# Kernel optimization log

Hardware: AMD Instinct MI355X
Metric: run time of the kernel (lower is better)

Reference implementation:

```python
import jax, jax.numpy as jnp
import numpy as np

D = 1024
H = 16
DH = D // H  # 64

def setup_inputs() -> dict:
    key = jax.random.key(0)
    ks = jax.random.split(key, 9)
    B, L = 2, 2048
    s = 1.0 / np.sqrt(D)
    inp = {
        'x':  jax.random.normal(ks[0], (B, L, D), dtype=jnp.float32),
        'Wq': jax.random.uniform(ks[1], (D, D), jnp.float32, -s, s),
        'bq': jnp.zeros((D,), jnp.float32),
        'Wk': jax.random.uniform(ks[2], (D, D), jnp.float32, -s, s),
        'bk': jnp.zeros((D,), jnp.float32),
        'Wv': jax.random.uniform(ks[3], (D, D), jnp.float32, -s, s),
        'bv': jnp.zeros((D,), jnp.float32),
        'Wo': jax.random.uniform(ks[4], (D, D), jnp.float32, -s, s),
        'bo': jnp.zeros((D,), jnp.float32),
    }
    return inp

def reference(x, Wq, bq, Wk, bk, Wv, bv, Wo, bo):
    B, L, _ = x.shape
    # projections (torch Linear: x @ W.T + b; here weights stored as [D_in, D_out])
    q = (x @ Wq + bq).reshape(B, L, H, DH).transpose(0, 2, 1, 3)  # [B,H,L,DH]
    k = (x @ Wk + bk).reshape(B, L, H, DH).transpose(0, 2, 1, 3)
    v = (x @ Wv + bv).reshape(B, L, H, DH).transpose(0, 2, 1, 3)
    scores = jnp.einsum('bhqd,bhkd->bhqk', q, k) / jnp.sqrt(jnp.float32(DH))
    attn = jax.nn.softmax(scores, axis=-1)  # dropout p=0 / eval -> identity
    out = jnp.einsum('bhqk,bhkd->bhqd', attn, v)
    out = out.transpose(0, 2, 1, 3).reshape(B, L, D)
    return out @ Wo + bo
```

## Files before the change

kernel.cpp:

```cpp
#include <hip/hip_runtime.h>
#include <stdint.h>

typedef __attribute__((ext_vector_type(8)))  __bf16 bf16x8;
typedef __attribute__((ext_vector_type(4)))  __bf16 bf16x4;
typedef __attribute__((ext_vector_type(4)))  float  f32x4;
typedef __attribute__((ext_vector_type(16))) float  f32x16;
typedef __attribute__((ext_vector_type(4)))  int    i32x4;

#define DEV static __device__ __forceinline__

DEV float fast_exp2(float x) {
#if __has_builtin(__builtin_amdgcn_exp2f)
  return __builtin_amdgcn_exp2f(x);
#else
  return exp2f(x);
#endif
}

DEV uint32_t pack_bf2(float a, float b) {
  __bf16 x = (__bf16)a, y = (__bf16)b;
  uint16_t xu = __builtin_bit_cast(uint16_t, x);
  uint16_t yu = __builtin_bit_cast(uint16_t, y);
  return (uint32_t)xu | ((uint32_t)yu << 16);
}

DEV void gload_lds16(const void* g, void* l) {
  __builtin_amdgcn_global_load_lds(
      (const __attribute__((address_space(1))) void*)(uintptr_t)(g),
      (__attribute__((address_space(3))) void*)(uint32_t)(uintptr_t)(l),
      16, 0, 0);
}

#define SM_SCALE 0.18033688f

__global__ void k_prep(const float* __restrict__ x,  __bf16* __restrict__ xb,
                       const float* __restrict__ Wq, const float* __restrict__ Wk,
                       const float* __restrict__ Wv, const float* __restrict__ Wo,
                       __bf16* __restrict__ wtq, __bf16* __restrict__ wot) {
  const int z = blockIdx.z;
  if (z < 4) {
    const float* W  = (z == 0) ? Wq : (z == 1) ? Wk : (z == 2) ? Wv : Wo;
    __bf16*      Wt = (z == 3) ? wot : (wtq + (size_t)z * 1024 * 1024);
    __shared__ __bf16 T[64][66];
    int t = threadIdx.x;
    int r = t >> 2;
    int cq = (t & 3) << 4;
    {
      int gk = blockIdx.y * 64 + r;
      int gn0 = blockIdx.x * 64 + cq;
      const float* src = W + (size_t)gk * 1024 + gn0;
#pragma unroll
      for (int j = 0; j < 16; j += 4) {
        f32x4 v = *(const f32x4*)(src + j);
#pragma unroll
        for (int jj = 0; jj < 4; ++jj) T[r][cq + j + jj] = (__bf16)v[jj];
      }
    }
    __syncthreads();
    {
      int gn = blockIdx.x * 64 + r;
      int gk0 = blockIdx.y * 64 + cq;
      __bf16* dst = Wt + (size_t)gn * 1024 + gk0;
      bf16x8 o0, o1;
#pragma unroll
      for (int j = 0; j < 8; ++j) { o0[j] = T[cq + j][r]; o1[j] = T[cq + 8 + j][r]; }
      *(bf16x8*)dst = o0;
      *(bf16x8*)(dst + 8) = o1;
    }
  } else {
    int lb = (z - 4) * 256 + blockIdx.y * 16 + blockIdx.x;
    int i = (lb * 256 + (int)threadIdx.x) * 4;
    if (i < 4096 * 1024) {
      f32x4 v = *(const f32x4*)(x + i);
      bf16x4 o;
      o[0] = (__bf16)v[0]; o[1] = (__bf16)v[1];
      o[2] = (__bf16)v[2]; o[3] = (__bf16)v[3];
      *(bf16x4*)(xb + i) = o;
    }
  }
}

__global__ void k_vt(const __bf16* __restrict__ qkv, __bf16* __restrict__ kvf) {
  int lt = blockIdx.x, bh = blockIdx.y;
  int b = bh >> 4, h = bh & 15;
  int t = threadIdx.x;
  int lane = t & 63, slot = t >> 6;
  int l31 = lane & 31, hi = lane >> 5;

  __shared__ __bf16 T[64][66];
  {
    int r = t >> 2, cq = (t & 3) << 4;
    const __bf16* src = qkv + (size_t)(b * 2048 + lt * 64 + r) * 3072 + 2048 + h * 64 + cq;
    bf16x8 v0 = *(const bf16x8*)src;
    bf16x8 v1 = *(const bf16x8*)(src + 8);
#pragma unroll
    for (int j = 0; j < 8; ++j) { T[r][cq + j] = v0[j]; T[r][cq + 8 + j] = v1[j]; }
  }
  __syncthreads();
#pragma unroll
  for (int tt = 0; tt < 2; ++tt) {
    bf16x8 val;
#pragma unroll
    for (int j = 0; j < 8; ++j)
      val[j] = T[tt * 32 + ((slot >> 1) * 2 + hi) * 8 + j][(slot & 1) * 32 + l31];
    __bf16* dst = kvf + (size_t)(bh * 64 + lt * 2 + tt) * 4096 + 2048 + slot * 512 + lane * 8;
    *(bf16x8*)dst = val;
  }
}

__global__ void k_gemm0(const __bf16* __restrict__ A, const __bf16* __restrict__ Bt,
                        __bf16* __restrict__ Cout, __bf16* __restrict__ kvf,
                        int M, int N, int K,
                        const float* __restrict__ b0, const float* __restrict__ b1,
                        const float* __restrict__ b2) {
  __shared__ __align__(16) __bf16 As[128 * 64];
  __shared__ __align__(16) __bf16 Bs[128 * 64];
  const int t = threadIdx.x, wid = t >> 6, lane = t & 63;
  const int f = blockIdx.x;
  const int xcd = f & 7, i = f >> 3;
  const int bm = (xcd & 3) * 8 + (i & 7);
  const int bn = (xcd >> 2) * 12 + (i >> 3);
  const int wm = wid >> 1, wn = wid & 1;
  const int l15 = lane & 15, l4 = lane >> 4;
  const int rr = lane >> 3, cc = lane & 7;
  f32x4 acc[4][4] = {};
  const int nk = K >> 6;
  for (int kt = 0; kt < nk; ++kt) {
    __syncthreads();
#pragma unroll
    for (int j = 0; j < 4; ++j) {
      int row = wid * 32 + j * 8 + rr;
      int csrc = (cc ^ (row & 7)) * 8;
      gload_lds16(A + (size_t)(bm * 128 + row) * K + kt * 64 + csrc,
                  (char*)As + (wid * 32 + j * 8) * 128);
      gload_lds16(Bt + (size_t)(bn * 128 + row) * K + kt * 64 + csrc,
                  (char*)Bs + (wid * 32 + j * 8) * 128);
    }
    __syncthreads();
#pragma unroll
    for (int kk = 0; kk < 2; ++kk) {
      bf16x8 a[4], b[4];
#pragma unroll
      for (int ms = 0; ms < 4; ++ms) {
        int row = wm * 64 + ms * 16 + l15;
        a[ms] = *(const bf16x8*)((char*)As + row * 128 + (((kk * 4 + l4) ^ (row & 7)) * 16));
      }
#pragma unroll
      for (int ns = 0; ns < 4; ++ns) {
        int row = wn * 64 + ns * 16 + l15;
        b[ns] = *(const bf16x8*)((char*)Bs + row * 128 + (((kk * 4 + l4) ^ (row & 7)) * 16));
      }
#pragma unroll
      for (int ms = 0; ms < 4; ++ms)
#pragma unroll
        for (int ns = 0; ns < 4; ++ns)
          acc[ms][ns] = __builtin_amdgcn_mfma_f32_16x16x32_bf16(a[ms], b[ns], acc[ms][ns], 0, 0, 0);
    }
  }
  const bool kblock = (bn >= 8 && bn < 16);
#pragma unroll
  for (int ms = 0; ms < 4; ++ms) {
#pragma unroll
    for (int ns = 0; ns < 4; ++ns) {
      int n = bn * 128 + wn * 64 + ns * 16 + l15;
      const float* bp = (n < 1024) ? b0 : ((n < 2048) ? b1 : b2);
      float bias = bp[n & 1023];
#pragma unroll
      for (int i2 = 0; i2 < 4; ++i2) {
        int m = bm * 128 + wm * 64 + ms * 16 + l4 * 4 + i2;
        float v = acc[ms][ns][i2] + bias;
        if (kblock) {
          int dfull = n - 1024;
          int h = dfull >> 6, d = dfull & 63;
          int bb = m >> 11, mr = m & 2047;
          int tile = mr >> 5, r32 = mr & 31;
          int lanep = r32 + ((d >> 3) & 1) * 32;
          kvf[(size_t)((bb * 16 + h) * 64 + tile) * 4096 +
              (d >> 4) * 512 + lanep * 8 + (d & 7)] = (__bf16)v;
        } else {
          if (n < 1024) v *= SM_SCALE;
          Cout[(size_t)m * N + n] = (__bf16)v;
        }
      }
    }
  }
}

__global__ void k_gemm1(const __bf16* __restrict__ A, const __bf16* __restrict__ Bt,
                        float* __restrict__ Cout, int M, int N, int K,
                        const float* __restrict__ b0) {
  __shared__ __align__(16) __bf16 As[128 * 64];
  __shared__ __align__(16) __bf16 Bs[64 * 64];
  const int t = threadIdx.x, wid = t >> 6, lane = t & 63;
  const int bm = blockIdx.y, bn = blockIdx.x;
  const int wm = wid >> 1, wn = wid & 1;
  const int l15 = lane & 15, l4 = lane >> 4;
  const int rr = lane >> 3, cc = lane & 7;
  f32x4 acc[4][2] = {};
  const int nk = K >> 6;
  for (int kt = 0; kt < nk; ++kt) {
    __syncthreads();
#pragma unroll
    for (int j = 0; j < 4; ++j) {
      int row = wid * 32 + j * 8 + rr;
      int csrc = (cc ^ (row & 7)) * 8;
      gload_lds16(A + (size_t)(bm * 128 + row) * K + kt * 64 + csrc,
                  (char*)As + (wid * 32 + j * 8) * 128);
    }
#pragma unroll
    for (int j = 0; j < 2; ++j) {
      int row = wid * 16 + j * 8 + rr;
      int csrc = (cc ^ (row & 7)) * 8;
      gload_lds16(Bt + (size_t)(bn * 64 + row) * K + kt * 64 + csrc,
                  (char*)Bs + (wid * 16 + j * 8) * 128);
    }
    __syncthreads();
#pragma unroll
    for (int kk = 0; kk < 2; ++kk) {
      bf16x8 a[4], b[2];
#pragma unroll
      for (int ms = 0; ms < 4; ++ms) {
        int row = wm * 64 + ms * 16 + l15;
        a[ms] = *(const bf16x8*)((char*)As + row * 128 + (((kk * 4 + l4) ^ (row & 7)) * 16));
      }
#pragma unroll
      for (int ns = 0; ns < 2; ++ns) {
        int row = wn * 32 + ns * 16 + l15;
        b[ns] = *(const bf16x8*)((char*)Bs + row * 128 + (((kk * 4 + l4) ^ (row & 7)) * 16));
      }
#pragma unroll
      for (int ms = 0; ms < 4; ++ms)
#pragma unroll
        for (int ns = 0; ns < 2; ++ns)
          acc[ms][ns] = __builtin_amdgcn_mfma_f32_16x16x32_bf16(a[ms], b[ns], acc[ms][ns], 0, 0, 0);
    }
  }
#pragma unroll
  for (int ms = 0; ms < 4; ++ms) {
#pragma unroll
    for (int ns = 0; ns < 2; ++ns) {
      int n = bn * 64 + wn * 32 + ns * 16 + l15;
      float bias = b0[n];
#pragma unroll
      for (int i = 0; i < 4; ++i) {
        int m = bm * 128 + wm * 64 + ms * 16 + l4 * 4 + i;
        Cout[(size_t)m * N + n] = acc[ms][ns][i] + bias;
      }
    }
  }
}

__global__ void __launch_bounds__(256, 2)
k_attn(const __bf16* __restrict__ qkv, const __bf16* __restrict__ kvf,
       __bf16* __restrict__ Aout) {
  __shared__ __align__(16) char smem[33792];
  const int t = threadIdx.x, w = t >> 6, lane = t & 63;
  const int qpair = w & 1, half = w >> 1;
  const int l31 = lane & 31, hi = lane >> 5;
  const int f = blockIdx.x;
  const int qt = (f >> 3) & 15;
  const int bh = (f & 7) + 8 * (f >> 7);
  const int b = bh >> 4, h = bh & 15;

  const char* kvbase = (const char*)kvf + (size_t)(bh * 64 + half * 32) * 8192 + lane * 16;

  bf16x8 aqA[4], aqB[4];
  {
    int qrow = b * 2048 + qt * 128 + qpair * 64 + l31;
    const __bf16* qp = qkv + (size_t)qrow * 3072 + h * 64 + hi * 8;
#pragma unroll
    for (int d = 0; d < 4; ++d) aqA[d] = *(const bf16x8*)(qp + d * 16);
    qp += (size_t)32 * 3072;
#pragma unroll
    for (int d = 0; d < 4; ++d) aqB[d] = *(const bf16x8*)(qp + d * 16);
  }

  f32x16 oA[2] = {}, oB[2] = {};
  float lsA = 0.f, lsB = 0.f;

  bf16x8 kA[4], vA[4], kB[4], vB[4];

  auto LOAD = [&](bf16x8* kf, bf16x8* vf, int tl) {
    const char* p = kvbase + (size_t)tl * 8192;
#pragma unroll
    for (int i = 0; i < 4; ++i) kf[i] = *(const bf16x8*)(p + i * 1024);
#pragma unroll
    for (int i = 0; i < 4; ++i) vf[i] = *(const bf16x8*)(p + 4096 + i * 1024);
  };

  auto BODY = [&](const bf16x8* kf, const bf16x8* vf, const bf16x8* aq,
                  f32x16* o, float& lsum) {
    f32x16 s;
    s = 0.f;
    __builtin_amdgcn_s_setprio(1);
#pragma unroll
    for (int d = 0; d < 4; ++d)
      s = __builtin_amdgcn_mfma_f32_32x32x16_bf16(kf[d], aq[d], s, 0, 0, 0);
    __builtin_amdgcn_s_setprio(0);

#pragma unroll
    for (int r = 0; r < 16; ++r) s[r] = fast_exp2(s[r]);

    float u[8];
#pragma unroll
    for (int c = 0; c < 8; ++c) u[c] = s[2 * c] + s[2 * c + 1];
#pragma unroll
    for (int st = 4; st > 0; st >>= 1)
#pragma unroll
      for (int c = 0; c < st; ++c) u[c] += u[c + st];
    lsum += u[0];

    uint32_t W[8];
#pragma unroll
    for (int c = 0; c < 8; ++c) W[c] = pack_bf2(s[2 * c], s[2 * c + 1]);

    bf16x8 pa[2];
#pragma unroll
    for (int kstep = 0; kstep < 2; ++kstep) {
      const int base = 4 * kstep;
      uint32_t w0 = W[base + 0], w1 = W[base + 1];
      uint32_t w2 = W[base + 2], w3 = W[base + 3];
      uint32_t x0 = __shfl_xor((int)w0, 32);
      uint32_t x1 = __shfl_xor((int)w1, 32);
      uint32_t x2 = __shfl_xor((int)w2, 32);
      uint32_t x3 = __shfl_xor((int)w3, 32);
      i32x4 pw;
      pw[0] = (int)(hi ? x2 : w0);
      pw[1] = (int)(hi ? x3 : w1);
      pw[2] = (int)(hi ? w2 : x0);
      pw[3] = (int)(hi ? w3 : x1);
      pa[kstep] = __builtin_bit_cast(bf16x8, pw);
    }

    __builtin_amdgcn_s_setprio(1);
#pragma unroll
    for (int kstep = 0; kstep < 2; ++kstep)
#pragma unroll
      for (int db = 0; db < 2; ++db)
        o[db] = __builtin_amdgcn_mfma_f32_32x32x16_bf16(pa[kstep], vf[kstep * 2 + db], o[db], 0, 0, 0);
    __builtin_amdgcn_s_setprio(0);
  };

  LOAD(kA, vA, 0);
  for (int tl = 0; tl < 32; tl += 2) {
    LOAD(kB, vB, tl + 1);
    BODY(kA, vA, aqA, oA, lsA);
    BODY(kA, vA, aqB, oB, lsB);
    if (tl + 2 < 32) LOAD(kA, vA, tl + 2);
    BODY(kB, vB, aqA, oA, lsA);
    BODY(kB, vB, aqB, oB, lsB);
  }

  lsA += __shfl_xor(lsA, 32);
  lsB += __shfl_xor(lsB, 32);

  float* oLDS = (float*)smem;
  float* sLDS = (float*)(smem + 32768);
  if (half == 1) {
    float* obA = oLDS + (qpair * 2 + 0) * 2048;
    float* obB = oLDS + (qpair * 2 + 1) * 2048;
#pragma unroll
    for (int db = 0; db < 2; ++db)
#pragma unroll
      for (int r = 0; r < 16; ++r) {
        obA[(db * 16 + r) * 64 + lane] = oA[db][r];
        obB[(db * 16 + r) * 64 + lane] = oB[db][r];
      }
    sLDS[(qpair * 2 + 0) * 64 + lane] = lsA;
    sLDS[(qpair * 2 + 1) * 64 + lane] = lsB;
  }
  __syncthreads();
  if (half == 0) {
    const float* obA = oLDS + (qpair * 2 + 0) * 2048;
    const float* obB = oLDS + (qpair * 2 + 1) * 2048;
#pragma unroll
    for (int db = 0; db < 2; ++db)
#pragma unroll
      for (int r = 0; r < 16; ++r) {
        oA[db][r] += obA[(db * 16 + r) * 64 + lane];
        oB[db][r] += obB[(db * 16 + r) * 64 + lane];
      }
    lsA += sLDS[(qpair * 2 + 0) * 64 + lane];
    lsB += sLDS[(qpair * 2 + 1) * 64 + lane];

    int qbase = b * 2048 + qt * 128 + qpair * 64;
#pragma unroll
    for (int r = 0; r < 16; ++r) {
      int rowq = (r & 3) + 8 * (r >> 2) + 4 * hi;
      float invA = 1.0f / __shfl(lsA, rowq);
      float invB = 1.0f / __shfl(lsB, rowq);
#pragma unroll
      for (int db = 0; db < 2; ++db) {
        int col = h * 64 + db * 32 + l31;
        Aout[(size_t)(qbase + rowq) * 1024 + col]      = (__bf16)(oA[db][r] * invA);
        Aout[(size_t)(qbase + 32 + rowq) * 1024 + col] = (__bf16)(oB[db][r] * invB);
      }
    }
  }
}

extern "C" void kernel_launch(void* const* d_in, const int* in_sizes, int n_in,
                              void* d_out, int out_size, void* d_ws, size_t ws_size,
                              hipStream_t stream) {
  const float* x  = (const float*)d_in[0];
  const float* Wq = (const float*)d_in[1];
  const float* bq = (const float*)d_in[2];
  const float* Wk = (const float*)d_in[3];
  const float* bk = (const float*)d_in[4];
  const float* Wv = (const float*)d_in[5];
  const float* bv = (const float*)d_in[6];
  const float* Wo = (const float*)d_in[7];
  const float* bo = (const float*)d_in[8];
  float* out = (float*)d_out;

  char* ws = (char*)d_ws;
  __bf16* xb   = (__bf16*)(ws);
  __bf16* aout = (__bf16*)(ws);
  __bf16* wtq  = (__bf16*)(ws + (8ull  << 20));
  __bf16* wot  = (__bf16*)(ws + (14ull << 20));
  __bf16* qkv  = (__bf16*)(ws + (16ull << 20));
  __bf16* kvf  = (__bf16*)(ws + (40ull << 20));

  k_prep<<<dim3(16, 16, 20), 256, 0, stream>>>(x, xb, Wq, Wk, Wv, Wo, wtq, wot);

  k_gemm0<<<dim3(768), 256, 0, stream>>>(xb, wtq, qkv, kvf, 4096, 3072, 1024, bq, bk, bv);

  k_vt<<<dim3(32, 32), 256, 0, stream>>>(qkv, kvf);

  k_attn<<<dim3(512), 256, 0, stream>>>(qkv, kvf, aout);

  k_gemm1<<<dim3(16, 32), 256, 0, stream>>>(aout, wot, out, 4096, 1024, 1024, bo);
}
```

Measured before the change: 110.8 us.

## Pre-swizzle QKV GEMM operands into MFMA fragment layout and load directly to registers

The prep kernel now writes x and the Q/K/V weights in a blocked layout that matches the MFMA 16x16x32 operand fragments, so each lane's 16-byte chunk is contiguous. The QKV GEMM drops its LDS staging and barriers and instead loads fragments straight from global memory, double-buffered in registers across k-steps, with launch bounds set for two blocks per CU. This removes LDS traffic and block-level synchronisation. In exchange, waves sharing the same A or B tiles now each fetch them from global memory or cache instead of sharing one LDS copy, and register pressure rises.

```diff
diff --git a/kernel.cpp b/kernel.cpp
--- a/kernel.cpp
+++ b/kernel.cpp
@@ -33,14 +33,14 @@
 
 #define SM_SCALE 0.18033688f
 
-__global__ void k_prep(const float* __restrict__ x,  __bf16* __restrict__ xb,
+
+__global__ void k_prep(const float* __restrict__ x,  __bf16* __restrict__ xf,
                        const float* __restrict__ Wq, const float* __restrict__ Wk,
                        const float* __restrict__ Wv, const float* __restrict__ Wo,
-                       __bf16* __restrict__ wtq, __bf16* __restrict__ wot) {
+                       __bf16* __restrict__ wf, __bf16* __restrict__ wot) {
   const int z = blockIdx.z;
   if (z < 4) {
-    const float* W  = (z == 0) ? Wq : (z == 1) ? Wk : (z == 2) ? Wv : Wo;
-    __bf16*      Wt = (z == 3) ? wot : (wtq + (size_t)z * 1024 * 1024);
+    const float* W = (z == 0) ? Wq : (z == 1) ? Wk : (z == 2) ? Wv : Wo;
     __shared__ __bf16 T[64][66];
     int t = threadIdx.x;
     int r = t >> 2;
@@ -57,26 +57,35 @@
       }
     }
     __syncthreads();
-    {
-      int gn = blockIdx.x * 64 + r;
-      int gk0 = blockIdx.y * 64 + cq;
-      __bf16* dst = Wt + (size_t)gn * 1024 + gk0;
-      bf16x8 o0, o1;
-#pragma unroll
-      for (int j = 0; j < 8; ++j) { o0[j] = T[cq + j][r]; o1[j] = T[cq + 8 + j][r]; }
+    int gn = blockIdx.x * 64 + r;
+    bf16x8 o0, o1;
+#pragma unroll
+    for (int j = 0; j < 8; ++j) { o0[j] = T[cq + j][r]; o1[j] = T[cq + 8 + j][r]; }
+    if (z == 3) {
+      __bf16* dst = wot + (size_t)gn * 1024 + blockIdx.y * 64 + cq;
       *(bf16x8*)dst = o0;
       *(bf16x8*)(dst + 8) = o1;
+    } else {
+      int nb = z * 64 + (gn >> 4);
+      int kb = blockIdx.y * 2 + (cq >= 32);
+      int lane0 = (gn & 15) + 16 * ((cq >> 3) & 3);
+      int lane1 = (gn & 15) + 16 * (((cq + 8) >> 3) & 3);
+      __bf16* blk = wf + ((size_t)nb * 32 + kb) * 512;
+      *(bf16x8*)(blk + lane0 * 8) = o0;
+      *(bf16x8*)(blk + lane1 * 8) = o1;
     }
   } else {
     int lb = (z - 4) * 256 + blockIdx.y * 16 + blockIdx.x;
-    int i = (lb * 256 + (int)threadIdx.x) * 4;
-    if (i < 4096 * 1024) {
-      f32x4 v = *(const f32x4*)(x + i);
-      bf16x4 o;
-      o[0] = (__bf16)v[0]; o[1] = (__bf16)v[1];
-      o[2] = (__bf16)v[2]; o[3] = (__bf16)v[3];
-      *(bf16x4*)(xb + i) = o;
-    }
+    int e = (lb * 256 + (int)threadIdx.x) * 8;
+    int m = e >> 10, k = e & 1023;
+    const float* src = x + (size_t)m * 1024 + k;
+    f32x4 v0 = *(const f32x4*)(src);
+    f32x4 v1 = *(const f32x4*)(src + 4);
+    bf16x8 o;
+#pragma unroll
+    for (int j = 0; j < 4; ++j) { o[j] = (__bf16)v0[j]; o[4 + j] = (__bf16)v1[j]; }
+    *(bf16x8*)(xf + ((size_t)(m >> 4) * 32 + (k >> 5)) * 512 +
+               ((m & 15) + 16 * ((k >> 3) & 3)) * 8) = o;
   }
 }
 
@@ -108,13 +117,11 @@
   }
 }
 
-__global__ void k_gemm0(const __bf16* __restrict__ A, const __bf16* __restrict__ Bt,
-                        __bf16* __restrict__ Cout, __bf16* __restrict__ kvf,
-                        int M, int N, int K,
-                        const float* __restrict__ b0, const float* __restrict__ b1,
-                        const float* __restrict__ b2) {
-  __shared__ __align__(16) __bf16 As[128 * 64];
-  __shared__ __align__(16) __bf16 Bs[128 * 64];
+__global__ void __launch_bounds__(256, 2)
+k_gemm0(const __bf16* __restrict__ xf, const __bf16* __restrict__ wf,
+        __bf16* __restrict__ Cout, __bf16* __restrict__ kvf,
+        const float* __restrict__ b0, const float* __restrict__ b1,
+        const float* __restrict__ b2) {
   const int t = threadIdx.x, wid = t >> 6, lane = t & 63;
   const int f = blockIdx.x;
   const int xcd = f & 7, i = f >> 3;
@@ -122,41 +129,41 @@
   const int bn = (xcd >> 2) * 12 + (i >> 3);
   const int wm = wid >> 1, wn = wid & 1;
   const int l15 = lane & 15, l4 = lane >> 4;
-  const int rr = lane >> 3, cc = lane & 7;
+
+  const char* abase = (const char*)xf + (size_t)(bm * 8 + wm * 4) * 32768 + lane * 16;
+  const char* bbase = (const char*)wf + (size_t)(bn * 8 + wn * 4) * 32768 + lane * 16;
+
   f32x4 acc[4][4] = {};
-  const int nk = K >> 6;
-  for (int kt = 0; kt < nk; ++kt) {
-    __syncthreads();
-#pragma unroll
-    for (int j = 0; j < 4; ++j) {
-      int row = wid * 32 + j * 8 + rr;
-      int csrc = (cc ^ (row & 7)) * 8;
-      gload_lds16(A + (size_t)(bm * 128 + row) * K + kt * 64 + csrc,
-                  (char*)As + (wid * 32 + j * 8) * 128);
-      gload_lds16(Bt + (size_t)(bn * 128 + row) * K + kt * 64 + csrc,
-                  (char*)Bs + (wid * 32 + j * 8) * 128);
-    }
-    __syncthreads();
-#pragma unroll
-    for (int kk = 0; kk < 2; ++kk) {
-      bf16x8 a[4], b[4];
-#pragma unroll
-      for (int ms = 0; ms < 4; ++ms) {
-        int row = wm * 64 + ms * 16 + l15;
-        a[ms] = *(const bf16x8*)((char*)As + row * 128 + (((kk * 4 + l4) ^ (row & 7)) * 16));
-      }
-#pragma unroll
-      for (int ns = 0; ns < 4; ++ns) {
-        int row = wn * 64 + ns * 16 + l15;
-        b[ns] = *(const bf16x8*)((char*)Bs + row * 128 + (((kk * 4 + l4) ^ (row & 7)) * 16));
-      }
+  bf16x8 aA[8], bA[8], aB[8], bB[8];
+
+  auto LOADF = [&](bf16x8* af, bf16x8* bf, int kt) {
+#pragma unroll
+    for (int kk = 0; kk < 2; ++kk)
+#pragma unroll
+      for (int s = 0; s < 4; ++s) {
+        af[kk * 4 + s] = *(const bf16x8*)(abase + s * 32768 + (kt * 2 + kk) * 1024);
+        bf[kk * 4 + s] = *(const bf16x8*)(bbase + s * 32768 + (kt * 2 + kk) * 1024);
+      }
+  };
+  auto STEP = [&](const bf16x8* af, const bf16x8* bf) {
+#pragma unroll
+    for (int kk = 0; kk < 2; ++kk)
 #pragma unroll
       for (int ms = 0; ms < 4; ++ms)
 #pragma unroll
         for (int ns = 0; ns < 4; ++ns)
-          acc[ms][ns] = __builtin_amdgcn_mfma_f32_16x16x32_bf16(a[ms], b[ns], acc[ms][ns], 0, 0, 0);
-    }
-  }
+          acc[ms][ns] = __builtin_amdgcn_mfma_f32_16x16x32_bf16(
+              af[kk * 4 + ms], bf[kk * 4 + ns], acc[ms][ns], 0, 0, 0);
+  };
+
+  LOADF(aA, bA, 0);
+  for (int kt = 0; kt < 16; kt += 2) {
+    LOADF(aB, bB, kt + 1);
+    STEP(aA, bA);
+    if (kt + 2 < 16) LOADF(aA, bA, kt + 2);
+    STEP(aB, bB);
+  }
+
   const bool kblock = (bn >= 8 && bn < 16);
 #pragma unroll
   for (int ms = 0; ms < 4; ++ms) {
@@ -179,7 +186,7 @@
               (d >> 4) * 512 + lanep * 8 + (d & 7)] = (__bf16)v;
         } else {
           if (n < 1024) v *= SM_SCALE;
-          Cout[(size_t)m * N + n] = (__bf16)v;
+          Cout[(size_t)m * 3072 + n] = (__bf16)v;
         }
       }
     }
@@ -414,16 +421,16 @@
   float* out = (float*)d_out;
 
   char* ws = (char*)d_ws;
-  __bf16* xb   = (__bf16*)(ws);
+  __bf16* xf   = (__bf16*)(ws);
   __bf16* aout = (__bf16*)(ws);
-  __bf16* wtq  = (__bf16*)(ws + (8ull  << 20));
+  __bf16* wf   = (__bf16*)(ws + (8ull  << 20));
   __bf16* wot  = (__bf16*)(ws + (14ull << 20));
   __bf16* qkv  = (__bf16*)(ws + (16ull << 20));
   __bf16* kvf  = (__bf16*)(ws + (40ull << 20));
 
-  k_prep<<<dim3(16, 16, 20), 256, 0, stream>>>(x, xb, Wq, Wk, Wv, Wo, wtq, wot);
-
-  k_gemm0<<<dim3(768), 256, 0, stream>>>(xb, wtq, qkv, kvf, 4096, 3072, 1024, bq, bk, bv);
+  k_prep<<<dim3(16, 16, 12), 256, 0, stream>>>(x, xf, Wq, Wk, Wv, Wo, wf, wot);
+
+  k_gemm0<<<dim3(768), 256, 0, stream>>>(xf, wf, qkv, kvf, bq, bk, bv);
 
   k_vt<<<dim3(32, 32), 256, 0, stream>>>(qkv, kvf);
 
```

After: 144.1 us. +30.1%, slower.
